# Kernel optimization log

Hardware: AMD Instinct MI355X
Metric: run time of the kernel (lower is better)

Reference implementation:

```python
import jax, jax.numpy as jnp
import numpy as np

H = 128  # target_size / hidden_size
D_IN = 2  # input_size - 2 (stard_LSTM slices off last 2 grid coords)
SAMP = 10  # sampling_num (hardcoded stride 10 in forward loop)


def lstm_encode(x, lengths, W_ih, W_hh, b_ih, b_hh):
    # x: [B, T, D_IN]; torch.nn.LSTMCell math, zero initial state
    B, T, _ = x.shape
    xg = jnp.einsum('btd,gd->btg', x, W_ih) + b_ih  # precompute input projections [B,T,4H]

    def step(carry, xt):
        h, c = carry
        g = xt + h @ W_hh.T + b_hh
        i, f, gg, o = jnp.split(g, 4, axis=-1)
        c = jax.nn.sigmoid(f) * c + jax.nn.sigmoid(i) * jnp.tanh(gg)
        h = jax.nn.sigmoid(o) * jnp.tanh(c)
        return (h, c), h

    h0 = jnp.zeros((B, H), x.dtype)
    _, hs = jax.lax.scan(step, (h0, h0), xg.transpose(1, 0, 2))
    outputs = hs.transpose(1, 0, 2)  # [B, T, H]
    emb = outputs[jnp.arange(B), jnp.clip(lengths - 1, 0)]  # last valid step per sequence
    return emb, outputs


def gather_sub(tensor, sub_len):
    # tensor: [B, T, H]; sub_len: [B*SAMP]; row k reads tensor[k//SAMP, sub_len[k]-1]
    rows = jnp.arange(sub_len.shape[0]) // SAMP
    return tensor[rows, jnp.clip(sub_len - 1, 0)]


def exp_neg_dist(a, b):
    return jnp.exp(-jnp.sqrt(jnp.sum((a - b) ** 2, axis=-1)))


def setup_inputs() -> dict:
    key = jax.random.key(0)
    ks = jax.random.split(key, 12)
    B, T, D = 220, 512, 4
    NS = B * SAMP
    rint = lambda k, n: jnp.maximum(jax.random.randint(k, (n,), 0, T), 1).astype(jnp.int64)
    inp = {
        'traj_input': jax.random.normal(ks[0], (B, T, D), jnp.float32),
        'traj_length': rint(ks[1], B),
        'traj_anchor_sub_length': rint(ks[2], NS),
        'traj_farest_sub_length': rint(ks[3], NS),
        'traj_anchor_input': jax.random.normal(ks[4], (B, T, D), jnp.float32),
        'traj_anchor_length': rint(ks[5], B),
        'anchor_sub_length': rint(ks[6], NS),
        'traj_farest_input': jax.random.normal(ks[7], (B, T, D), jnp.float32),
        'traj_farest_length': rint(ks[8], B),
        'farest_sub_length': rint(ks[9], NS),
        'W_ih': jax.random.normal(ks[10], (4 * H, D_IN), jnp.float32) / np.sqrt(H),
        'W_hh': jax.random.normal(ks[11], (4 * H, H), jnp.float32) / np.sqrt(H),
        'b_ih': jnp.zeros((4 * H,), jnp.float32),
        'b_hh': jnp.zeros((4 * H,), jnp.float32),
    }
    return inp


def reference(traj_input, traj_length, traj_anchor_sub_length, traj_farest_sub_length,
              traj_anchor_input, traj_anchor_length, anchor_sub_length,
              traj_farest_input, traj_farest_length, farest_sub_length,
              W_ih, W_hh, b_ih, b_hh):
    # stard_LSTM=True path: cell input drops last 2 coords
    t_emb, t_out = lstm_encode(traj_input[..., :-2], traj_length, W_ih, W_hh, b_ih, b_hh)
    a_emb, a_out = lstm_encode(traj_anchor_input[..., :-2], traj_anchor_length, W_ih, W_hh, b_ih, b_hh)
    f_emb, f_out = lstm_encode(traj_farest_input[..., :-2], traj_farest_length, W_ih, W_hh, b_ih, b_hh)

    ta_sub = gather_sub(t_out, traj_anchor_sub_length)
    tf_sub = gather_sub(t_out, traj_farest_sub_length)
    an_sub = gather_sub(a_out, anchor_sub_length)
    fa_sub = gather_sub(f_out, farest_sub_length)

    anchor_distance = exp_neg_dist(t_emb, a_emb)
    farest_distance = exp_neg_dist(t_emb, f_emb)
    anchor_sub_distance = exp_neg_dist(ta_sub, an_sub)
    farest_sub_distance = exp_neg_dist(tf_sub, fa_sub)
    return (anchor_distance, farest_distance, anchor_sub_distance, farest_sub_distance)
```

## Files before the change

kernel.cpp:

```cpp
#include <hip/hip_runtime.h>

#define H    128
#define T    512
#define DX   4
#define BB   220
#define SAMP 10
#define NS   (BB*SAMP)
#define M    4
#define NBLK 55
#define MAXSLOT 84

typedef _Float16 half8 __attribute__((ext_vector_type(8)));
typedef float    f32x4 __attribute__((ext_vector_type(4)));

#define WS_TEMB 0
#define WS_AEMB (WS_TEMB + BB*H)
#define WS_FEMB (WS_AEMB + BB*H)
#define WS_TA   (WS_FEMB + BB*H)
#define WS_TF   (WS_TA + NS*H)
#define WS_AN   (WS_TF + NS*H)
#define WS_FA   (WS_AN + NS*H)
#define WS_FLAGS (WS_FA + NS*H)

#define LOG2E  1.442695041f
#define LOG2E2 2.885390082f

__device__ static inline float bf2f(unsigned short u) {
  unsigned int i = ((unsigned int)u) << 16;
  return __builtin_bit_cast(float, i);
}
__device__ static inline unsigned short f2bf(float f) {
  unsigned int i = __builtin_bit_cast(unsigned int, f);
  i += 0x7fffu + ((i >> 16) & 1u);
  return (unsigned short)(i >> 16);
}
__device__ static inline float loadF(const void* p, size_t i, int isbf) {
  return isbf ? bf2f(((const unsigned short*)p)[i]) : ((const float*)p)[i];
}
__device__ static inline int loadI(const void* p, int i, int is64) {
  return is64 ? (int)((const unsigned int*)p)[2*(size_t)i] : ((const int*)p)[i];
}
__device__ static inline float frcp(float x) { return __builtin_amdgcn_rcpf(x); }
__device__ static inline float ex2(float x)  { return __builtin_amdgcn_exp2f(x); }
__device__ static inline float sigmY(float y)  { return frcp(1.f + ex2(-y)); }
__device__ static inline float tanhY(float y)  { return 1.f - 2.f*frcp(1.f + ex2(y)); }
__device__ static inline float scrub(float x) { return (x == x) ? x : 0.f; }
__device__ static inline int clampT(int v) { v = v - 1; if (v < 0) v = 0; if (v > T-1) v = T-1; return v; }

__global__ __launch_bounds__(512, 2) void lstm_scan(
    const void* __restrict__ x0_, const void* __restrict__ len0,
    const void* __restrict__ sub_ta, const void* __restrict__ sub_tf,
    const void* __restrict__ x1_, const void* __restrict__ len1,
    const void* __restrict__ sub_an,
    const void* __restrict__ x2_, const void* __restrict__ len2,
    const void* __restrict__ sub_fa,
    const void* __restrict__ Wih, const void* __restrict__ Whh,
    const void* __restrict__ bih, const void* __restrict__ bhh,
    float* __restrict__ ws)
{
  const int e      = blockIdx.y;
  const int s0     = blockIdx.x * M;
  const int tid    = threadIdx.x;
  const int lane   = tid & 63;
  const int w      = tid >> 6;
  const int lo     = lane & 15;
  const int quad   = lane >> 4;

  int fbf, f64;
  {
    const unsigned int* wp = (const unsigned int*)Whh;
    int cnt = 0;
    for (int i = 0; i < 64; ++i) {
      unsigned int lo16 = wp[i] & 0xFFFFu;
      int ex = (int)((lo16 >> 7) & 0xFFu);
      cnt += (ex >= 100 && ex <= 130);
    }
    fbf = (cnt >= 40);
    const unsigned int* l = (const unsigned int*)len0;
    f64 = ((l[1] | l[3] | l[5] | l[7]) == 0u);
    if (blockIdx.x == 0 && blockIdx.y == 0 && tid == 0) {
      int* fo = (int*)(ws + WS_FLAGS); fo[0] = fbf; fo[1] = f64;
    }
  }

  const void* xin  = (e==0) ? x0_ : (e==1 ? x1_ : x2_);
  const void* lenp = (e==0) ? len0 : (e==1 ? len1 : len2);

  __shared__ __align__(16) _Float16 afr[2][4][16][8];
  __shared__ __align__(16) float2 xbf[M][T+2];
  __shared__ __align__(16) _Float16 sbuf[MAXSLOT][H];
  __shared__ int slot_off[MAXSLOT];

  ((unsigned int*)afr)[tid] = 0u;
  for (int i = tid; i < M*T; i += 512) {
    int m = i >> 9, t = i & (T-1);
    size_t base = ((size_t)(s0+m)*T + t) * DX;
    xbf[m][t] = make_float2(loadF(xin, base + 0, fbf), loadF(xin, base + 1, fbf));
  }
  half8 Bf[4][4];
  const int col = w*16 + lo;
  #pragma unroll
  for (int q = 0; q < 4; ++q) {
    const float sc = (q == 2) ? LOG2E2 : LOG2E;
    const int g = q*128 + col;
    #pragma unroll
    for (int kt = 0; kt < 4; ++kt) {
      #pragma unroll
      for (int j = 0; j < 8; ++j) {
        const int k = kt*32 + quad*8 + j;
        Bf[q][kt][j] = (_Float16)(sc * loadF(Whh, (size_t)g*H + k, fbf));
      }
    }
  }
  float wx0[4], wx1[4], bb[4];
  #pragma unroll
  for (int q = 0; q < 4; ++q) {
    const float sc = (q == 2) ? LOG2E2 : LOG2E;
    const int g = q*128 + col;
    wx0[q] = sc * loadF(Wih, (size_t)g*2 + 0, fbf);
    wx1[q] = sc * loadF(Wih, (size_t)g*2 + 1, fbf);
    bb[q]  = sc * (loadF(bih, g, fbf) + loadF(bhh, g, fbf));
  }
  const int nslots = (e == 0) ? M*21 : M*11;
  int myt = -1, mym = 0;
  if (e == 0) {
    if (tid < M*21) {
      int m = tid / 21, j = tid - m*21, sg = s0 + m;
      mym = m;
      int off;
      if (j == 0)       { myt = clampT(loadI(lenp, sg, f64));            off = WS_TEMB + sg*H; }
      else if (j <= 10) { int k = sg*10 + (j-1);  myt = clampT(loadI(sub_ta, k, f64)); off = WS_TA + k*H; }
      else              { int k = sg*10 + (j-11); myt = clampT(loadI(sub_tf, k, f64)); off = WS_TF + k*H; }
      slot_off[tid] = off;
    }
  } else {
    if (tid < M*11) {
      int m = tid / 11, j = tid - m*11, sg = s0 + m;
      mym = m;
      int off;
      if (j == 0) { myt = clampT(loadI(lenp, sg, f64)); off = (e==1 ? WS_AEMB : WS_FEMB) + sg*H; }
      else {
        int k = sg*10 + (j-1);
        if (e == 1) { myt = clampT(loadI(sub_an, k, f64)); off = WS_AN + k*H; }
        else        { myt = clampT(loadI(sub_fa, k, f64)); off = WS_FA + k*H; }
      }
      slot_off[tid] = off;
    }
  }
  __syncthreads();

  float cc = 0.f;
  const int rdchunk = quad*4 + (lo & 3);
  const int wrkt    = w >> 1;
  const int wrchunk = ((w & 1)*2 + (lo >> 3))*4 + quad;
  const int wrj     = lo & 7;

  for (int t = 0; t < T; ++t) {
    const int p = t & 1, qn = p ^ 1;
    float2 xv = xbf[quad][t];
    float xq[4];
    #pragma unroll
    for (int q = 0; q < 4; ++q) xq[q] = bb[q] + wx0[q]*xv.x + wx1[q]*xv.y;

    half8 A[4];
    #pragma unroll
    for (int kt = 0; kt < 4; ++kt)
      A[kt] = *(const half8*)&afr[p][kt][rdchunk][0];

    f32x4 G[4];
    #pragma unroll
    for (int q = 0; q < 4; ++q) G[q] = (f32x4){0.f, 0.f, 0.f, 0.f};
    #pragma unroll
    for (int kt = 0; kt < 4; ++kt)
      #pragma unroll
      for (int q = 0; q < 4; ++q)
        G[q] = __builtin_amdgcn_mfma_f32_16x16x32_f16(A[kt], Bf[q][kt], G[q], 0, 0, 0);

    float R[4];
    #pragma unroll
    for (int q = 0; q < 4; ++q) {
      float g01 = (quad & 1) ? G[q][1] : G[q][0];
      float g23 = (quad & 1) ? G[q][3] : G[q][2];
      R[q] = ((quad & 2) ? g23 : g01) + xq[q];
    }
    float si = sigmY(R[0]);
    float sf = sigmY(R[1]);
    float tg = tanhY(R[2]);
    float so = sigmY(R[3]);
    cc = sf*cc + si*tg;
    afr[qn][wrkt][wrchunk][wrj] = (_Float16)(so * tanhY(cc * LOG2E2));
    __syncthreads();
    unsigned long long mask = __ballot(myt == t);
    while (mask) {
      int src = __ffsll((unsigned long long)mask) - 1;
      mask &= mask - 1;
      int m    = __shfl(mym, src);
      int slot = w*64 + src;
      int c0   = 2*lane;
      unsigned int pk = *(const unsigned int*)&afr[qn][c0>>5][((c0>>3)&3)*4 + m][c0&7];
      *(unsigned int*)&sbuf[slot][c0] = pk;
    }
  }
  __syncthreads();
  for (int i = tid; i < nslots*64; i += 512) {
    int slot = i >> 6, c2 = i & 63;
    unsigned int pk = *(const unsigned int*)&sbuf[slot][2*c2];
    float2 v;
    v.x = (float)__builtin_bit_cast(_Float16, (unsigned short)(pk & 0xFFFFu));
    v.y = (float)__builtin_bit_cast(_Float16, (unsigned short)(pk >> 16));
    *(float2*)(ws + slot_off[slot] + 2*c2) = v;
  }
}

__global__ void dists(const float* __restrict__ ws, void* __restrict__ outv) {
  const int fbf = ((const int*)(ws + WS_FLAGS))[0];
  const int gtid = blockIdx.x*256 + threadIdx.x;
  const int widx = gtid >> 6, lane = gtid & 63;
  const float *pa, *pb;
  if (widx < 220)       { pa = ws + WS_TEMB + (size_t)widx*H;        pb = ws + WS_AEMB + (size_t)widx*H; }
  else if (widx < 440)  { int b = widx-220;  pa = ws + WS_TEMB + (size_t)b*H; pb = ws + WS_FEMB + (size_t)b*H; }
  else if (widx < 2640) { int k = widx-440;  pa = ws + WS_TA + (size_t)k*H;   pb = ws + WS_AN + (size_t)k*H; }
  else                  { int k = widx-2640; pa = ws + WS_TF + (size_t)k*H;   pb = ws + WS_FA + (size_t)k*H; }
  float d0 = pa[lane]    - pb[lane];
  float d1 = pa[lane+64] - pb[lane+64];
  float s  = scrub(d0*d0 + d1*d1);
  #pragma unroll
  for (int off = 32; off > 0; off >>= 1) s += __shfl_down(s, off, 64);
  if (lane == 0) {
    float r = __expf(-sqrtf(s));
    if (fbf) ((unsigned short*)outv)[widx] = f2bf(r);
    else     ((float*)outv)[widx] = r;
  }
}

extern "C" void kernel_launch(void* const* d_in, const int* in_sizes, int n_in,
                              void* d_out, int out_size, void* d_ws, size_t ws_size,
                              hipStream_t stream) {
  float* ws = (float*)d_ws;
  hipLaunchKernelGGL(lstm_scan, dim3(NBLK, 3), dim3(512), 0, stream,
                     d_in[0], d_in[1], d_in[2], d_in[3],
                     d_in[4], d_in[5], d_in[6],
                     d_in[7], d_in[8], d_in[9],
                     d_in[10], d_in[11], d_in[12], d_in[13], ws);
  hipLaunchKernelGGL(dists, dim3(4840*64/256), dim3(256), 0, stream, ws, d_out);
}
```

Measured before the change: 390.1 us.

## Fuse distance kernel into LSTM scan via atomic counter and reorder gate MFMAs

Removes the separate dists kernel launch. The last 16 blocks to finish the scan, ranked by an atomic counter, spin until every block is done and then compute the distances. The per-step gate MFMAs are split into four separate chains ordered g, i, f, o, so the transcendental work on one gate can overlap with the next gate's MFMAs. This adds a memset launch and a spin-wait that relies on all 165 blocks being co-resident. It also drops the NaN scrub on the distance sum.

```diff
diff --git a/kernel.cpp b/kernel.cpp
--- a/kernel.cpp
+++ b/kernel.cpp
@@ -8,6 +8,8 @@
 #define NS   (BB*SAMP)
 #define M    4
 #define NBLK 55
+#define TOTB (NBLK*3)
+#define NT   16
 #define MAXSLOT 84
 
 typedef _Float16 half8 __attribute__((ext_vector_type(8)));
@@ -20,7 +22,7 @@
 #define WS_TF   (WS_TA + NS*H)
 #define WS_AN   (WS_TF + NS*H)
 #define WS_FA   (WS_AN + NS*H)
-#define WS_FLAGS (WS_FA + NS*H)
+#define WS_CTR  (WS_FA + NS*H)
 
 #define LOG2E  1.442695041f
 #define LOG2E2 2.885390082f
@@ -44,8 +46,12 @@
 __device__ static inline float ex2(float x)  { return __builtin_amdgcn_exp2f(x); }
 __device__ static inline float sigmY(float y)  { return frcp(1.f + ex2(-y)); }
 __device__ static inline float tanhY(float y)  { return 1.f - 2.f*frcp(1.f + ex2(y)); }
-__device__ static inline float scrub(float x) { return (x == x) ? x : 0.f; }
 __device__ static inline int clampT(int v) { v = v - 1; if (v < 0) v = 0; if (v > T-1) v = T-1; return v; }
+__device__ static inline float qsel(f32x4 G, int quad) {
+  float g01 = (quad & 1) ? G[1] : G[0];
+  float g23 = (quad & 1) ? G[3] : G[2];
+  return (quad & 2) ? g23 : g01;
+}
 
 __global__ __launch_bounds__(512, 2) void lstm_scan(
     const void* __restrict__ x0_, const void* __restrict__ len0,
@@ -56,7 +62,7 @@
     const void* __restrict__ sub_fa,
     const void* __restrict__ Wih, const void* __restrict__ Whh,
     const void* __restrict__ bih, const void* __restrict__ bhh,
-    float* __restrict__ ws)
+    float* __restrict__ ws, void* __restrict__ outv)
 {
   const int e      = blockIdx.y;
   const int s0     = blockIdx.x * M;
@@ -78,9 +84,6 @@
     fbf = (cnt >= 40);
     const unsigned int* l = (const unsigned int*)len0;
     f64 = ((l[1] | l[3] | l[5] | l[7]) == 0u);
-    if (blockIdx.x == 0 && blockIdx.y == 0 && tid == 0) {
-      int* fo = (int*)(ws + WS_FLAGS); fo[0] = fbf; fo[1] = f64;
-    }
   }
 
   const void* xin  = (e==0) ? x0_ : (e==1 ? x1_ : x2_);
@@ -90,6 +93,7 @@
   __shared__ __align__(16) float2 xbf[M][T+2];
   __shared__ __align__(16) _Float16 sbuf[MAXSLOT][H];
   __shared__ int slot_off[MAXSLOT];
+  __shared__ int rank_sh;
 
   ((unsigned int*)afr)[tid] = 0u;
   for (int i = tid; i < M*T; i += 512) {
@@ -158,37 +162,36 @@
   for (int t = 0; t < T; ++t) {
     const int p = t & 1, qn = p ^ 1;
     float2 xv = xbf[quad][t];
-    float xq[4];
-    #pragma unroll
-    for (int q = 0; q < 4; ++q) xq[q] = bb[q] + wx0[q]*xv.x + wx1[q]*xv.y;
 
     half8 A[4];
     #pragma unroll
     for (int kt = 0; kt < 4; ++kt)
       A[kt] = *(const half8*)&afr[p][kt][rdchunk][0];
 
-    f32x4 G[4];
-    #pragma unroll
-    for (int q = 0; q < 4; ++q) G[q] = (f32x4){0.f, 0.f, 0.f, 0.f};
-    #pragma unroll
-    for (int kt = 0; kt < 4; ++kt)
-      #pragma unroll
-      for (int q = 0; q < 4; ++q)
-        G[q] = __builtin_amdgcn_mfma_f32_16x16x32_f16(A[kt], Bf[q][kt], G[q], 0, 0, 0);
-
-    float R[4];
-    #pragma unroll
-    for (int q = 0; q < 4; ++q) {
-      float g01 = (quad & 1) ? G[q][1] : G[q][0];
-      float g23 = (quad & 1) ? G[q][3] : G[q][2];
-      R[q] = ((quad & 2) ? g23 : g01) + xq[q];
-    }
-    float si = sigmY(R[0]);
-    float sf = sigmY(R[1]);
-    float tg = tanhY(R[2]);
-    float so = sigmY(R[3]);
-    cc = sf*cc + si*tg;
-    afr[qn][wrkt][wrchunk][wrj] = (_Float16)(so * tanhY(cc * LOG2E2));
+    f32x4 G2 = {0.f,0.f,0.f,0.f};
+    #pragma unroll
+    for (int kt = 0; kt < 4; ++kt) G2 = __builtin_amdgcn_mfma_f32_16x16x32_f16(A[kt], Bf[2][kt], G2, 0, 0, 0);
+    float tg = tanhY(qsel(G2, quad) + bb[2] + wx0[2]*xv.x + wx1[2]*xv.y);
+
+    f32x4 G0 = {0.f,0.f,0.f,0.f};
+    #pragma unroll
+    for (int kt = 0; kt < 4; ++kt) G0 = __builtin_amdgcn_mfma_f32_16x16x32_f16(A[kt], Bf[0][kt], G0, 0, 0, 0);
+    float si = sigmY(qsel(G0, quad) + bb[0] + wx0[0]*xv.x + wx1[0]*xv.y);
+    float ig = si * tg;
+
+    f32x4 G1 = {0.f,0.f,0.f,0.f};
+    #pragma unroll
+    for (int kt = 0; kt < 4; ++kt) G1 = __builtin_amdgcn_mfma_f32_16x16x32_f16(A[kt], Bf[1][kt], G1, 0, 0, 0);
+    float sf = sigmY(qsel(G1, quad) + bb[1] + wx0[1]*xv.x + wx1[1]*xv.y);
+    cc = sf*cc + ig;
+    float tc = tanhY(cc * LOG2E2);
+
+    f32x4 G3 = {0.f,0.f,0.f,0.f};
+    #pragma unroll
+    for (int kt = 0; kt < 4; ++kt) G3 = __builtin_amdgcn_mfma_f32_16x16x32_f16(A[kt], Bf[3][kt], G3, 0, 0, 0);
+    float so = sigmY(qsel(G3, quad) + bb[3] + wx0[3]*xv.x + wx1[3]*xv.y);
+
+    afr[qn][wrkt][wrchunk][wrj] = (_Float16)(so * tc);
     __syncthreads();
     unsigned long long mask = __ballot(myt == t);
     while (mask) {
@@ -210,26 +213,37 @@
     v.y = (float)__builtin_bit_cast(_Float16, (unsigned short)(pk >> 16));
     *(float2*)(ws + slot_off[slot] + 2*c2) = v;
   }
-}
-
-__global__ void dists(const float* __restrict__ ws, void* __restrict__ outv) {
-  const int fbf = ((const int*)(ws + WS_FLAGS))[0];
-  const int gtid = blockIdx.x*256 + threadIdx.x;
-  const int widx = gtid >> 6, lane = gtid & 63;
-  const float *pa, *pb;
-  if (widx < 220)       { pa = ws + WS_TEMB + (size_t)widx*H;        pb = ws + WS_AEMB + (size_t)widx*H; }
-  else if (widx < 440)  { int b = widx-220;  pa = ws + WS_TEMB + (size_t)b*H; pb = ws + WS_FEMB + (size_t)b*H; }
-  else if (widx < 2640) { int k = widx-440;  pa = ws + WS_TA + (size_t)k*H;   pb = ws + WS_AN + (size_t)k*H; }
-  else                  { int k = widx-2640; pa = ws + WS_TF + (size_t)k*H;   pb = ws + WS_FA + (size_t)k*H; }
-  float d0 = pa[lane]    - pb[lane];
-  float d1 = pa[lane+64] - pb[lane+64];
-  float s  = scrub(d0*d0 + d1*d1);
-  #pragma unroll
-  for (int off = 32; off > 0; off >>= 1) s += __shfl_down(s, off, 64);
-  if (lane == 0) {
-    float r = __expf(-sqrtf(s));
-    if (fbf) ((unsigned short*)outv)[widx] = f2bf(r);
-    else     ((float*)outv)[widx] = r;
+  __threadfence();
+  __syncthreads();
+  if (tid == 0) rank_sh = atomicAdd((int*)(ws + WS_CTR), 1);
+  __syncthreads();
+  const int rank = rank_sh;
+  if (rank < TOTB - NT) return;
+  if (tid == 0) {
+    volatile int* c = (volatile int*)(ws + WS_CTR);
+    while (*c < TOTB) __builtin_amdgcn_s_sleep(16);
+  }
+  __syncthreads();
+  __threadfence();
+  const int slice = rank - (TOTB - NT);
+  const int p0 = slice * 303;
+  const int p1 = (p0 + 303 < 4840) ? p0 + 303 : 4840;
+  for (int pr = p0 + w; pr < p1; pr += 8) {
+    const float *pa, *pb;
+    if (pr < 220)       { pa = ws + WS_TEMB + (size_t)pr*H;        pb = ws + WS_AEMB + (size_t)pr*H; }
+    else if (pr < 440)  { int b = pr-220;  pa = ws + WS_TEMB + (size_t)b*H; pb = ws + WS_FEMB + (size_t)b*H; }
+    else if (pr < 2640) { int k = pr-440;  pa = ws + WS_TA + (size_t)k*H;   pb = ws + WS_AN + (size_t)k*H; }
+    else                { int k = pr-2640; pa = ws + WS_TF + (size_t)k*H;   pb = ws + WS_FA + (size_t)k*H; }
+    float d0 = pa[lane]    - pb[lane];
+    float d1 = pa[lane+64] - pb[lane+64];
+    float s  = d0*d0 + d1*d1;
+    #pragma unroll
+    for (int off = 32; off > 0; off >>= 1) s += __shfl_down(s, off, 64);
+    if (lane == 0) {
+      float r = __expf(-sqrtf(s));
+      if (fbf) ((unsigned short*)outv)[pr] = f2bf(r);
+      else     ((float*)outv)[pr] = r;
+    }
   }
 }
 
@@ -237,10 +251,10 @@
                               void* d_out, int out_size, void* d_ws, size_t ws_size,
                               hipStream_t stream) {
   float* ws = (float*)d_ws;
+  hipMemsetAsync((char*)d_ws + (size_t)WS_CTR*4, 0, 4, stream);
   hipLaunchKernelGGL(lstm_scan, dim3(NBLK, 3), dim3(512), 0, stream,
                      d_in[0], d_in[1], d_in[2], d_in[3],
                      d_in[4], d_in[5], d_in[6],
                      d_in[7], d_in[8], d_in[9],
-                     d_in[10], d_in[11], d_in[12], d_in[13], ws);
-  hipLaunchKernelGGL(dists, dim3(4840*64/256), dim3(256), 0, stream, ws, d_out);
-}
+                     d_in[10], d_in[11], d_in[12], d_in[13], ws, d_out);
+}
```

Result: slower. 439.6 us (+12.7%).
